# Optimization experiments

Measured on AMD Instinct MI355X. Metric: run time of the kernel, lower is better.

The kernel has to match this reference:

```python
import jax, jax.numpy as jnp
import numpy as np

HEAD_SIZE = 64
EMBED_DIM = 1024

def setup_inputs() -> dict:
    key = jax.random.key(0)
    kx, kq, kk, kv = jax.random.split(key, 4)
    B, T, C, H = 8, 2048, EMBED_DIM, HEAD_SIZE
    scale = 1.0 / np.sqrt(C)
    x = jax.random.normal(kx, (B, T, C), dtype=jnp.float32)
    # nn.Linear(C, H, bias=False): weight (H, C); store as (C, H) for x @ W
    Wq = jax.random.normal(kq, (C, H), dtype=jnp.float32) * scale
    Wk = jax.random.normal(kk, (C, H), dtype=jnp.float32) * scale
    Wv = jax.random.normal(kv, (C, H), dtype=jnp.float32) * scale
    return {"x": x, "Wq": Wq, "Wk": Wk, "Wv": Wv}

def reference(x, Wq, Wk, Wv):
    B, T, C = x.shape
    H = Wq.shape[1]
    q = x @ Wq  # (B, T, H)
    k = x @ Wk
    v = x @ Wv
    # scaled scores with causal mask (tril)
    wei = jnp.einsum('bth,bsh->bts', q, k) * (H ** -0.5)  # (B, T, T)
    causal = jnp.tril(jnp.ones((T, T), dtype=bool))
    wei = jnp.where(causal, wei, -jnp.inf)
    wei = jax.nn.softmax(wei, axis=-1)
    out = jnp.einsum('bts,bsh->bth', wei, v)  # (B, T, H)
    return out
```

## Files before the change

### kernel.cpp

```cpp
#include <hip/hip_runtime.h>

#define T_SEQ 2048
#define C_DIM 1024
#define H_DIM 64
#define B_DIM 8
#define NROW (B_DIM * T_SEQ)

typedef __attribute__((ext_vector_type(8))) short short8;
typedef __attribute__((ext_vector_type(4))) float f32x4;

__device__ __forceinline__ short f2bf(float f) {
  unsigned u = __builtin_bit_cast(unsigned, f);
  u += 0x7fffu + ((u >> 16) & 1u);
  return (short)(u >> 16);
}

__global__ __launch_bounds__(256) void w_transpose(
    const float* __restrict__ Wq, const float* __restrict__ Wk,
    const float* __restrict__ Wv, short* __restrict__ Wt) {
  __shared__ float tile[64][65];
  const int mat = blockIdx.x >> 4;
  const int k0 = (blockIdx.x & 15) * 64;
  const float* W = (mat == 0) ? Wq : (mat == 1 ? Wk : Wv);
  const int t = threadIdx.x;
#pragma unroll
  for (int i = 0; i < 16; ++i) {
    int idx = t + i * 256;
    int kk = idx >> 6, h = idx & 63;
    tile[kk][h] = W[(size_t)(k0 + kk) * H_DIM + h];
  }
  __syncthreads();
#pragma unroll
  for (int i = 0; i < 16; ++i) {
    int idx = t + i * 256;
    int h = idx >> 6, kk = idx & 63;
    Wt[((size_t)mat * 64 + h) * C_DIM + k0 + kk] = f2bf(tile[kk][h]);
  }
}

__device__ __forceinline__ int lds_addr(int tile, int kh, int qd, int nn) {
  return tile * 2048 + kh * 512 + (qd * 16 + (nn ^ ((kh * 4 + qd) & 7))) * 8;
}

__global__ __launch_bounds__(256) void qkv_gemm(
    const float* __restrict__ x, const short* __restrict__ Wt,
    short* __restrict__ q, short* __restrict__ k, short* __restrict__ vt) {
  __shared__ __align__(16) short As[4096];
  __shared__ __align__(16) short Bs[24576];
  const int tid = threadIdx.x;
  const int w = tid >> 6, lane = tid & 63;
  const int n16 = lane & 15, quad = lane >> 4;
  const int row0 = blockIdx.x * 32;

  f32x4 acc[2][3];
#pragma unroll
  for (int mt = 0; mt < 2; ++mt)
#pragma unroll
    for (int ln = 0; ln < 3; ++ln) acc[mt][ln] = (f32x4){0.f, 0.f, 0.f, 0.f};

  short8 bstg[12];
  float4 astg[2][2];

#pragma unroll
  for (int i = 0; i < 12; ++i) {
    const int u = i * 256 + tid, h = u >> 4, uk = u & 15;
    bstg[i] = *(const short8*)(Wt + (size_t)h * C_DIM + uk * 8);
  }
#pragma unroll
  for (int i = 0; i < 2; ++i) {
    const int u2 = i * 256 + tid, sr = u2 >> 4, f = u2 & 15;
    const float* ap = x + (size_t)(row0 + sr) * C_DIM + f * 8;
    astg[i][0] = *(const float4*)ap;
    astg[i][1] = *(const float4*)(ap + 4);
  }

  for (int kc = 0; kc < 8; ++kc) {
    __syncthreads();
#pragma unroll
    for (int i = 0; i < 12; ++i) {
      const int u = i * 256 + tid, h = u >> 4, uk = u & 15;
      *(short8*)(Bs + lds_addr(h >> 4, uk >> 2, uk & 3, h & 15)) = bstg[i];
    }
#pragma unroll
    for (int i = 0; i < 2; ++i) {
      const int u2 = i * 256 + tid, sr = u2 >> 4, f = u2 & 15;
      short8 av;
#pragma unroll
      for (int e = 0; e < 4; ++e) {
        av[e] = f2bf(((const float*)&astg[i][0])[e]);
        av[e + 4] = f2bf(((const float*)&astg[i][1])[e]);
      }
      *(short8*)(As + lds_addr(sr >> 4, f >> 2, f & 3, sr & 15)) = av;
    }
    __syncthreads();
    if (kc < 7) {
      const int k0n = (kc + 1) * 128;
#pragma unroll
      for (int i = 0; i < 12; ++i) {
        const int u = i * 256 + tid, h = u >> 4, uk = u & 15;
        bstg[i] = *(const short8*)(Wt + (size_t)h * C_DIM + k0n + uk * 8);
      }
#pragma unroll
      for (int i = 0; i < 2; ++i) {
        const int u2 = i * 256 + tid, sr = u2 >> 4, f = u2 & 15;
        const float* ap = x + (size_t)(row0 + sr) * C_DIM + k0n + f * 8;
        astg[i][0] = *(const float4*)ap;
        astg[i][1] = *(const float4*)(ap + 4);
      }
    }
#pragma unroll
    for (int kh = 0; kh < 4; ++kh) {
      short8 afr[2];
#pragma unroll
      for (int mt = 0; mt < 2; ++mt)
        afr[mt] = *(const short8*)(As + lds_addr(mt, kh, quad, n16));
#pragma unroll
      for (int ln = 0; ln < 3; ++ln) {
        const short8 bfr =
            *(const short8*)(Bs + lds_addr(w * 3 + ln, kh, quad, n16));
        acc[0][ln] =
            __builtin_amdgcn_mfma_f32_16x16x32_bf16(afr[0], bfr, acc[0][ln], 0, 0, 0);
        acc[1][ln] =
            __builtin_amdgcn_mfma_f32_16x16x32_bf16(afr[1], bfr, acc[1][ln], 0, 0, 0);
      }
    }
  }

  const int b = row0 >> 11;
#pragma unroll
  for (int mt = 0; mt < 2; ++mt)
#pragma unroll
    for (int ln = 0; ln < 3; ++ln) {
      const int ntg = w * 3 + ln;
      const int mat = ntg >> 2;
      const int cl = (ntg & 3) * 16 + n16;
#pragma unroll
      for (int r = 0; r < 4; ++r) {
        const int row = row0 + mt * 16 + quad * 4 + r;
        const float v = acc[mt][ln][r];
        if (mat == 0)
          q[(size_t)row * H_DIM + cl] = f2bf(v * 0.125f);
        else if (mat == 1)
          k[(size_t)row * H_DIM + cl] = f2bf(v);
        else
          vt[((size_t)b * H_DIM + cl) * T_SEQ + (row & (T_SEQ - 1))] = f2bf(v);
      }
    }
}

__global__ __launch_bounds__(256) void attn_mfma(
    const short* __restrict__ q, const short* __restrict__ k,
    const short* __restrict__ vt, float* __restrict__ out) {
  __shared__ __align__(16) short pbuf[4][1024];
  __shared__ __align__(16) float oshare[3][1024];
  __shared__ __align__(16) float lshare[3][256];
  const int tid = threadIdx.x;
  const int w = tid >> 6;
  const int lane = tid & 63;
  const int n16 = lane & 15, quad = lane >> 4;
  const int b = blockIdx.x & 7;
  const int qt = (T_SEQ / 16 - 1) - (blockIdx.x >> 3);
  const int r0 = qt * 16;

  const short* qb = q + ((size_t)b * T_SEQ + r0) * H_DIM;
  const short* kb = k + (size_t)b * T_SEQ * H_DIM;
  const short* vb = vt + (size_t)b * H_DIM * T_SEQ;

  const short8 aq0 = *(const short8*)(qb + (size_t)n16 * H_DIM + quad * 8);
  const short8 aq1 = *(const short8*)(qb + (size_t)n16 * H_DIM + 32 + quad * 8);

  f32x4 O[4];
#pragma unroll
  for (int i = 0; i < 4; ++i) O[i] = (f32x4){0.f, 0.f, 0.f, 0.f};
  float lsum[4] = {0.f, 0.f, 0.f, 0.f};

  const int nj = (r0 + 16 + 63) >> 6;
  for (int jt = w; jt < nj; jt += 4) {
    const int j0 = jt * 64;

    short8 bk[4][2];
#pragma unroll
    for (int nt = 0; nt < 4; ++nt) {
      const short* kp = kb + (size_t)(j0 + nt * 16 + n16) * H_DIM + quad * 8;
      bk[nt][0] = *(const short8*)kp;
      bk[nt][1] = *(const short8*)(kp + 32);
    }

    f32x4 s[4];
#pragma unroll
    for (int nt = 0; nt < 4; ++nt) {
      f32x4 z = (f32x4){0.f, 0.f, 0.f, 0.f};
      z = __builtin_amdgcn_mfma_f32_16x16x32_bf16(aq0, bk[nt][0], z, 0, 0, 0);
      z = __builtin_amdgcn_mfma_f32_16x16x32_bf16(aq1, bk[nt][1], z, 0, 0, 0);
      s[nt] = z;
    }

    const bool full = (j0 + 64 <= r0);
#pragma unroll
    for (int nt = 0; nt < 4; ++nt) {
      const int base =
          (nt >> 1) * 512 + ((((nt & 1) << 1) | (n16 >> 3)) * 128) + (n16 & 7);
#pragma unroll
      for (int r = 0; r < 4; ++r) {
        float p;
        if (full) {
          p = __expf(s[nt][r]);
        } else {
          const int j = j0 + nt * 16 + n16;
          const int row = r0 + quad * 4 + r;
          p = (j <= row) ? __expf(s[nt][r]) : 0.f;
        }
        lsum[r] += p;
        pbuf[w][base + (quad * 4 + r) * 8] = f2bf(p);
      }
    }

    short8 bv[4][2];
#pragma unroll
    for (int ht = 0; ht < 4; ++ht)
#pragma unroll
      for (int kh = 0; kh < 2; ++kh)
        bv[ht][kh] = *(const short8*)(vb + (size_t)(ht * 16 + n16) * T_SEQ +
                                      j0 + kh * 32 + quad * 8);

    const short8 ap0 = *(const short8*)(&pbuf[w][0] + lane * 8);
    const short8 ap1 = *(const short8*)(&pbuf[w][0] + 512 + lane * 8);

#pragma unroll
    for (int ht = 0; ht < 4; ++ht) {
      O[ht] = __builtin_amdgcn_mfma_f32_16x16x32_bf16(ap0, bv[ht][0], O[ht], 0, 0, 0);
      O[ht] = __builtin_amdgcn_mfma_f32_16x16x32_bf16(ap1, bv[ht][1], O[ht], 0, 0, 0);
    }
  }

  if (w != 0) {
#pragma unroll
    for (int ht = 0; ht < 4; ++ht)
#pragma unroll
      for (int r = 0; r < 4; ++r)
        oshare[w - 1][(ht * 4 + r) * 64 + lane] = O[ht][r];
#pragma unroll
    for (int r = 0; r < 4; ++r) lshare[w - 1][r * 64 + lane] = lsum[r];
  }
  __syncthreads();
  if (w == 0) {
#pragma unroll
    for (int ht = 0; ht < 4; ++ht)
#pragma unroll
      for (int r = 0; r < 4; ++r) {
        float a = O[ht][r];
#pragma unroll
        for (int ow = 0; ow < 3; ++ow) a += oshare[ow][(ht * 4 + r) * 64 + lane];
        O[ht][r] = a;
      }
#pragma unroll
    for (int r = 0; r < 4; ++r) {
      float vsum = lsum[r];
#pragma unroll
      for (int ow = 0; ow < 3; ++ow) vsum += lshare[ow][r * 64 + lane];
      vsum += __shfl_xor(vsum, 1);
      vsum += __shfl_xor(vsum, 2);
      vsum += __shfl_xor(vsum, 4);
      vsum += __shfl_xor(vsum, 8);
      lsum[r] = vsum;
    }
#pragma unroll
    for (int ht = 0; ht < 4; ++ht)
#pragma unroll
      for (int r = 0; r < 4; ++r)
        out[((size_t)b * T_SEQ + r0 + quad * 4 + r) * H_DIM + ht * 16 + n16] =
            O[ht][r] / lsum[r];
  }
}

extern "C" void kernel_launch(void* const* d_in, const int* in_sizes, int n_in,
                              void* d_out, int out_size, void* d_ws,
                              size_t ws_size, hipStream_t stream) {
  const float* x = (const float*)d_in[0];
  const float* Wq = (const float*)d_in[1];
  const float* Wk = (const float*)d_in[2];
  const float* Wv = (const float*)d_in[3];

  char* ws = (char*)d_ws;
  short* Wt = (short*)ws;
  short* q = (short*)(ws + 3 * 64 * 1024 * 2);
  short* kk = (short*)(ws + 3 * 64 * 1024 * 2 + 2097152);
  short* vt = (short*)(ws + 3 * 64 * 1024 * 2 + 2 * 2097152);

  w_transpose<<<48, 256, 0, stream>>>(Wq, Wk, Wv, Wt);
  qkv_gemm<<<NROW / 32, 256, 0, stream>>>(x, Wt, q, kk, vt);
  attn_mfma<<<B_DIM * (T_SEQ / 16), 256, 0, stream>>>(q, kk, vt, (float*)d_out);
}
```

Baseline: 143.4 us.

## Pre-swizzle weights into MFMA fragment order and double-buffer A in QKV GEMM

```diff
diff --git a/kernel.cpp b/kernel.cpp
--- a/kernel.cpp
+++ b/kernel.cpp
@@ -15,38 +15,35 @@
   return (short)(u >> 16);
 }
 
-__global__ __launch_bounds__(256) void w_transpose(
+__global__ __launch_bounds__(256) void w_prep(
     const float* __restrict__ Wq, const float* __restrict__ Wk,
-    const float* __restrict__ Wv, short* __restrict__ Wt) {
-  __shared__ float tile[64][65];
-  const int mat = blockIdx.x >> 4;
-  const int k0 = (blockIdx.x & 15) * 64;
+    const float* __restrict__ Wv, short* __restrict__ Wt2) {
+  const int unit = blockIdx.x * 256 + threadIdx.x;
+  const int lane = unit & 63;
+  const int t = unit >> 6;
+  const int kh = t & 3;
+  const int g = t >> 2;
+  const int ntg = g % 12;
+  const int kc = g / 12;
+  const int n16 = lane & 15, quad = lane >> 4;
+  const int mat = ntg >> 2;
+  const int h = (ntg & 3) * 16 + n16;
+  const int kb = kc * 128 + kh * 32 + quad * 8;
   const float* W = (mat == 0) ? Wq : (mat == 1 ? Wk : Wv);
-  const int t = threadIdx.x;
-#pragma unroll
-  for (int i = 0; i < 16; ++i) {
-    int idx = t + i * 256;
-    int kk = idx >> 6, h = idx & 63;
-    tile[kk][h] = W[(size_t)(k0 + kk) * H_DIM + h];
-  }
-  __syncthreads();
-#pragma unroll
-  for (int i = 0; i < 16; ++i) {
-    int idx = t + i * 256;
-    int h = idx >> 6, kk = idx & 63;
-    Wt[((size_t)mat * 64 + h) * C_DIM + k0 + kk] = f2bf(tile[kk][h]);
-  }
+  short8 v;
+#pragma unroll
+  for (int e = 0; e < 8; ++e) v[e] = f2bf(W[(size_t)(kb + e) * H_DIM + h]);
+  *(short8*)(Wt2 + (size_t)unit * 8) = v;
 }
 
 __device__ __forceinline__ int lds_addr(int tile, int kh, int qd, int nn) {
   return tile * 2048 + kh * 512 + (qd * 16 + (nn ^ ((kh * 4 + qd) & 7))) * 8;
 }
 
-__global__ __launch_bounds__(256) void qkv_gemm(
-    const float* __restrict__ x, const short* __restrict__ Wt,
+__global__ __launch_bounds__(256, 2) void qkv_gemm(
+    const float* __restrict__ x, const short* __restrict__ Wt2,
     short* __restrict__ q, short* __restrict__ k, short* __restrict__ vt) {
-  __shared__ __align__(16) short As[4096];
-  __shared__ __align__(16) short Bs[24576];
+  __shared__ __align__(16) short As[2][4096];
   const int tid = threadIdx.x;
   const int w = tid >> 6, lane = tid & 63;
   const int n16 = lane & 15, quad = lane >> 4;
@@ -58,73 +55,92 @@
 #pragma unroll
     for (int ln = 0; ln < 3; ++ln) acc[mt][ln] = (f32x4){0.f, 0.f, 0.f, 0.f};
 
-  short8 bstg[12];
-  float4 astg[2][2];
-
-#pragma unroll
-  for (int i = 0; i < 12; ++i) {
-    const int u = i * 256 + tid, h = u >> 4, uk = u & 15;
-    bstg[i] = *(const short8*)(Wt + (size_t)h * C_DIM + uk * 8);
-  }
-#pragma unroll
-  for (int i = 0; i < 2; ++i) {
-    const int u2 = i * 256 + tid, sr = u2 >> 4, f = u2 & 15;
-    const float* ap = x + (size_t)(row0 + sr) * C_DIM + f * 8;
-    astg[i][0] = *(const float4*)ap;
-    astg[i][1] = *(const float4*)(ap + 4);
-  }
-
+  const int u20 = tid, u21 = 256 + tid;
+  const int sr0 = u20 >> 4, f0 = u20 & 15;
+  const int sr1 = u21 >> 4, f1 = u21 & 15;
+  const float* ap0 = x + (size_t)(row0 + sr0) * C_DIM + f0 * 8;
+  const float* ap1 = x + (size_t)(row0 + sr1) * C_DIM + f1 * 8;
+  const int soff0 = lds_addr(sr0 >> 4, f0 >> 2, f0 & 3, sr0 & 15);
+  const int soff1 = lds_addr(sr1 >> 4, f1 >> 2, f1 & 3, sr1 & 15);
+
+  int swz[4];
+#pragma unroll
+  for (int kh = 0; kh < 4; ++kh)
+    swz[kh] = (quad * 16 + (n16 ^ ((kh * 4 + quad) & 7))) * 8;
+
+  const short* bbase = Wt2 + (size_t)(w * 3) * 2048 + (size_t)lane * 8;
+
+  float4 astg[2][4];
+  short8 bfr[12];
+
+#define STAGE_A(d, p)                                      \
+  {                                                        \
+    short8 av0, av1;                                       \
+    _Pragma("unroll") for (int e = 0; e < 4; ++e) {        \
+      av0[e] = f2bf(((const float*)&astg[d][0])[e]);       \
+      av0[e + 4] = f2bf(((const float*)&astg[d][1])[e]);   \
+      av1[e] = f2bf(((const float*)&astg[d][2])[e]);       \
+      av1[e + 4] = f2bf(((const float*)&astg[d][3])[e]);   \
+    }                                                      \
+    *(short8*)(&As[p][0] + soff0) = av0;                   \
+    *(short8*)(&As[p][0] + soff1) = av1;                   \
+  }
+
+  astg[0][0] = *(const float4*)(ap0);
+  astg[0][1] = *(const float4*)(ap0 + 4);
+  astg[0][2] = *(const float4*)(ap1);
+  astg[0][3] = *(const float4*)(ap1 + 4);
+  astg[1][0] = *(const float4*)(ap0 + 128);
+  astg[1][1] = *(const float4*)(ap0 + 132);
+  astg[1][2] = *(const float4*)(ap1 + 128);
+  astg[1][3] = *(const float4*)(ap1 + 132);
+#pragma unroll
+  for (int ln = 0; ln < 3; ++ln)
+#pragma unroll
+    for (int kh = 0; kh < 4; ++kh)
+      bfr[ln * 4 + kh] = *(const short8*)(bbase + ln * 2048 + kh * 512);
+  STAGE_A(0, 0);
+  asm volatile("s_waitcnt lgkmcnt(0)" ::: "memory");
+  __builtin_amdgcn_sched_barrier(0);
+  __builtin_amdgcn_s_barrier();
+  __builtin_amdgcn_sched_barrier(0);
+
+#pragma unroll
   for (int kc = 0; kc < 8; ++kc) {
-    __syncthreads();
-#pragma unroll
-    for (int i = 0; i < 12; ++i) {
-      const int u = i * 256 + tid, h = u >> 4, uk = u & 15;
-      *(short8*)(Bs + lds_addr(h >> 4, uk >> 2, uk & 3, h & 15)) = bstg[i];
-    }
-#pragma unroll
-    for (int i = 0; i < 2; ++i) {
-      const int u2 = i * 256 + tid, sr = u2 >> 4, f = u2 & 15;
-      short8 av;
-#pragma unroll
-      for (int e = 0; e < 4; ++e) {
-        av[e] = f2bf(((const float*)&astg[i][0])[e]);
-        av[e + 4] = f2bf(((const float*)&astg[i][1])[e]);
-      }
-      *(short8*)(As + lds_addr(sr >> 4, f >> 2, f & 3, sr & 15)) = av;
-    }
-    __syncthreads();
+    const short* asb = &As[kc & 1][0];
+#pragma unroll
+    for (int kh = 0; kh < 4; ++kh) {
+      const short8 a0 = *(const short8*)(asb + kh * 512 + swz[kh]);
+      const short8 a1 = *(const short8*)(asb + 2048 + kh * 512 + swz[kh]);
+#pragma unroll
+      for (int ln = 0; ln < 3; ++ln) {
+        acc[0][ln] = __builtin_amdgcn_mfma_f32_16x16x32_bf16(
+            a0, bfr[ln * 4 + kh], acc[0][ln], 0, 0, 0);
+        acc[1][ln] = __builtin_amdgcn_mfma_f32_16x16x32_bf16(
+            a1, bfr[ln * 4 + kh], acc[1][ln], 0, 0, 0);
+      }
+    }
     if (kc < 7) {
-      const int k0n = (kc + 1) * 128;
-#pragma unroll
-      for (int i = 0; i < 12; ++i) {
-        const int u = i * 256 + tid, h = u >> 4, uk = u & 15;
-        bstg[i] = *(const short8*)(Wt + (size_t)h * C_DIM + k0n + uk * 8);
-      }
-#pragma unroll
-      for (int i = 0; i < 2; ++i) {
-        const int u2 = i * 256 + tid, sr = u2 >> 4, f = u2 & 15;
-        const float* ap = x + (size_t)(row0 + sr) * C_DIM + k0n + f * 8;
-        astg[i][0] = *(const float4*)ap;
-        astg[i][1] = *(const float4*)(ap + 4);
-      }
-    }
-#pragma unroll
-    for (int kh = 0; kh < 4; ++kh) {
-      short8 afr[2];
-#pragma unroll
-      for (int mt = 0; mt < 2; ++mt)
-        afr[mt] = *(const short8*)(As + lds_addr(mt, kh, quad, n16));
-#pragma unroll
-      for (int ln = 0; ln < 3; ++ln) {
-        const short8 bfr =
-            *(const short8*)(Bs + lds_addr(w * 3 + ln, kh, quad, n16));
-        acc[0][ln] =
-            __builtin_amdgcn_mfma_f32_16x16x32_bf16(afr[0], bfr, acc[0][ln], 0, 0, 0);
-        acc[1][ln] =
-            __builtin_amdgcn_mfma_f32_16x16x32_bf16(afr[1], bfr, acc[1][ln], 0, 0, 0);
-      }
-    }
-  }
+      const short* bc = bbase + (size_t)(kc + 1) * 24576;
+#pragma unroll
+      for (int ln = 0; ln < 3; ++ln)
+#pragma unroll
+        for (int kh = 0; kh < 4; ++kh)
+          bfr[ln * 4 + kh] = *(const short8*)(bc + ln * 2048 + kh * 512);
+      if (kc < 6) {
+        astg[kc & 1][0] = *(const float4*)(ap0 + (kc + 2) * 128);
+        astg[kc & 1][1] = *(const float4*)(ap0 + (kc + 2) * 128 + 4);
+        astg[kc & 1][2] = *(const float4*)(ap1 + (kc + 2) * 128);
+        astg[kc & 1][3] = *(const float4*)(ap1 + (kc + 2) * 128 + 4);
+      }
+      STAGE_A((kc + 1) & 1, (kc + 1) & 1);
+      asm volatile("s_waitcnt lgkmcnt(0)" ::: "memory");
+      __builtin_amdgcn_sched_barrier(0);
+      __builtin_amdgcn_s_barrier();
+      __builtin_amdgcn_sched_barrier(0);
+    }
+  }
+#undef STAGE_A
 
   const int b = row0 >> 11;
 #pragma unroll
@@ -287,7 +303,7 @@
   short* kk = (short*)(ws + 3 * 64 * 1024 * 2 + 2097152);
   short* vt = (short*)(ws + 3 * 64 * 1024 * 2 + 2 * 2097152);
 
-  w_transpose<<<48, 256, 0, stream>>>(Wq, Wk, Wv, Wt);
+  w_prep<<<96, 256, 0, stream>>>(Wq, Wk, Wv, Wt);
   qkv_gemm<<<NROW / 32, 256, 0, stream>>>(x, Wt, q, kk, vt);
   attn_mfma<<<B_DIM * (T_SEQ / 16), 256, 0, stream>>>(q, kk, vt, (float*)d_out);
 }
```

After: 143.2 us. No clear change (-0.2%).
